# Performance work log

Hardware: AMD Instinct MI355X
Metric: run time of the kernel (lower is better)

## Reference

```python
import jax, jax.numpy as jnp
import numpy as np

B, L, D = 16, 2048, 1024  # memory_len == input_len (mask is applied on both axes)
NEG = -1e20


def setup_inputs() -> dict:
    key = jax.random.key(0)
    k1, k2, k3, k4, k5, k6 = jax.random.split(key, 6)
    inp = jax.random.normal(k1, (B, L, D), dtype=jnp.float32)
    mem = jax.random.normal(k2, (B, L, D), dtype=jnp.float32)
    # True = masked-out position; keep sparsity low so rows stay mostly valid
    mask = jax.random.bernoulli(k3, 0.1, (B, L))
    inv = 1.0 / np.sqrt(D)
    w_input = jax.random.normal(k4, (D,), dtype=jnp.float32) * inv   # Linear(D,1) weight
    w_memory = jax.random.normal(k5, (D,), dtype=jnp.float32) * inv  # Linear(D,1) weight
    dot_scale = jax.random.uniform(k6, (D,), dtype=jnp.float32, minval=0.0, maxval=inv)
    return {"input": inp, "memory": mem, "mask": mask,
            "w_input": w_input, "w_memory": w_memory, "dot_scale": dot_scale}


def reference(input, memory, mask, w_input, w_memory, dot_scale):
    # dropout p = 0.0 -> identity
    input_dot = jnp.einsum("bld,d->bl", input, w_input)[:, :, None]   # [B,L,1]
    memory_dot = jnp.einsum("bmd,d->bm", memory, w_memory)[:, None, :]  # [B,1,M]
    cross_dot = jnp.einsum("bld,bmd->blm", input * dot_scale, memory)   # [B,L,M]
    att = input_dot + memory_dot + cross_dot
    bad = mask[:, :, None] | mask[:, None, :]                           # [B,L,M]
    att = jnp.where(bad, NEG, att)
    weight_one = jax.nn.softmax(att, axis=-1)                           # over memory axis
    output_one = jnp.einsum("blm,bmd->bld", weight_one, memory)
    weight_two = jax.nn.softmax(att.max(axis=-1), axis=-1)[:, None, :]  # [B,1,L]
    output_two = jnp.einsum("bol,bld->bod", weight_two, input)          # [B,1,D]
    return jnp.concatenate(
        [input, output_one, input * output_one, output_two * output_one], axis=-1)
```

## Files before the change

### kernel.cpp

```cpp
#include <hip/hip_runtime.h>
#include <hip/hip_bf16.h>


#define BDIM 16
#define LDIM 2048
#define MDIM 2048
#define DDIM 1024
#define NEGF (-60000.0f)

typedef float    f32x4v __attribute__((ext_vector_type(4)));
typedef _Float16 half8  __attribute__((ext_vector_type(8)));
typedef _Float16 half4  __attribute__((ext_vector_type(4)));

#define GL16(gp, lp)                                                        \
  __builtin_amdgcn_global_load_lds(                                         \
      (const __attribute__((address_space(1))) unsigned int*)(gp),          \
      (__attribute__((address_space(3))) unsigned int*)(lp), 16, 0, 0)

__global__ __launch_bounds__(256) void conv_kernel(
    const float* __restrict__ input, const float* __restrict__ memory,
    const float* __restrict__ w_in, const float* __restrict__ w_mem,
    const float* __restrict__ scale,
    _Float16* __restrict__ Qh, _Float16* __restrict__ Kh,
    float* __restrict__ idot, float* __restrict__ mdot) {
  const int t = threadIdx.x, lane = t & 63, wid = t >> 6;
  const size_t row = (size_t)blockIdx.x * 4 + wid;
  const float* ir  = input  + row * DDIM;
  const float* mrp = memory + row * DDIM;
  float di = 0.f, dm = 0.f;
#pragma unroll
  for (int c = 0; c < 4; ++c) {
    const int off = c * 256 + lane * 4;
    float4 sc4 = *(const float4*)&scale[off];
    float4 wi4 = *(const float4*)&w_in[off];
    float4 wm4 = *(const float4*)&w_mem[off];
    float4 v = *(const float4*)&ir[off];
    di += v.x * wi4.x + v.y * wi4.y + v.z * wi4.z + v.w * wi4.w;
    half4 q = { (_Float16)(v.x * sc4.x), (_Float16)(v.y * sc4.y),
                (_Float16)(v.z * sc4.z), (_Float16)(v.w * sc4.w) };
    *(half4*)&Qh[row * DDIM + off] = q;
    float4 u = *(const float4*)&mrp[off];
    dm += u.x * wm4.x + u.y * wm4.y + u.z * wm4.z + u.w * wm4.w;
    half4 k = { (_Float16)u.x, (_Float16)u.y, (_Float16)u.z, (_Float16)u.w };
    *(half4*)&Kh[row * DDIM + off] = k;
  }
#pragma unroll
  for (int o = 1; o < 64; o <<= 1) {
    di += __shfl_xor(di, o, 64);
    dm += __shfl_xor(dm, o, 64);
  }
  if (lane == 0) { idot[row] = di; mdot[row] = dm; }
}

__global__ __launch_bounds__(256) void tr_kernel(const _Float16* __restrict__ Kh,
                                                 _Float16* __restrict__ Vt) {
  const int b = blockIdx.z;
  const int d0 = blockIdx.x * 64, m0 = blockIdx.y * 64;
  __shared__ _Float16 sT[64][80];
  const int t = threadIdx.x;
  {
    const int mr = t >> 2, ch = (t & 3) * 16;
    const _Float16* src = Kh + ((size_t)b * MDIM + m0 + mr) * DDIM + d0 + ch;
    *(half8*)&sT[mr][ch]     = *(const half8*)&src[0];
    *(half8*)&sT[mr][ch + 8] = *(const half8*)&src[8];
  }
  __syncthreads();
  {
    const int dr = t >> 2, mc = (t & 3) * 16;
    union { _Float16 h[16]; half8 v[2]; } tmp;
#pragma unroll
    for (int j = 0; j < 16; ++j) tmp.h[j] = sT[mc + j][dr];
    _Float16* dst = Vt + ((size_t)b * DDIM + d0 + dr) * MDIM + m0 + mc;
    *(half8*)&dst[0] = tmp.v[0];
    *(half8*)&dst[8] = tmp.v[1];
  }
}

__device__ __forceinline__ void stage128(const _Float16* __restrict__ Ab,
                                         const _Float16* __restrict__ Bb,
                                         _Float16* sAb, _Float16* sBb,
                                         int stride, int k0, int wid, int lane) {
  const int rsub = lane >> 3;
  const int sc = ((lane & 7) ^ rsub) * 8;
#pragma unroll
  for (int j = 0; j < 4; ++j) {
    const int r0 = wid * 32 + j * 8;
    const size_t go = (size_t)(r0 + rsub) * stride + k0 + sc;
    GL16(Ab + go, sAb + r0 * 64);
    GL16(Bb + go, sBb + r0 * 64);
  }
}

__device__ __forceinline__ void compute128(const _Float16* sAb, const _Float16* sBb,
                                           f32x4v acc[4][4], int wr, int wc,
                                           int lane) {
  const int l15 = lane & 15;
#pragma unroll
  for (int kk = 0; kk < 2; ++kk) {
    const int colh = ((kk * 4 + (lane >> 4)) ^ (lane & 7)) * 8;
    half8 aF[4], bF[4];
#pragma unroll
    for (int i = 0; i < 4; ++i) {
      aF[i] = *(const half8*)&sAb[(wr * 64 + i * 16 + l15) * 64 + colh];
      bF[i] = *(const half8*)&sBb[(wc * 64 + i * 16 + l15) * 64 + colh];
    }
#pragma unroll
    for (int mi = 0; mi < 4; ++mi)
#pragma unroll
      for (int ni = 0; ni < 4; ++ni)
        acc[mi][ni] = __builtin_amdgcn_mfma_f32_16x16x32_f16(aF[mi], bF[ni],
                                                             acc[mi][ni], 0, 0, 0);
  }
}

__global__ __launch_bounds__(256, 3) void gemm1_kernel(
    const _Float16* __restrict__ Qh, const _Float16* __restrict__ Kh,
    const float* __restrict__ idot, const float* __restrict__ mdot,
    const int* __restrict__ mask, _Float16* __restrict__ Sp) {
  const int id = blockIdx.x;
  const int wg = (id & 7) * 512 + (id >> 3);
  const int b = wg >> 8, rem = wg & 255, by = rem >> 4, bx = rem & 15;
  const int t = threadIdx.x, lane = t & 63, wid = t >> 6;
  const int wr = wid >> 1, wc = wid & 1;
  __shared__ _Float16 sA[128 * 64];
  __shared__ _Float16 sB[128 * 64];
  __shared__ float s_dl[128], s_dm[128];
  __shared__ int   s_ml[128], s_mm[128];
  if (t < 128) {
    s_dl[t] = idot[b * LDIM + by * 128 + t];
    s_ml[t] = mask[b * LDIM + by * 128 + t];
    s_dm[t] = mdot[b * MDIM + bx * 128 + t];
    s_mm[t] = mask[b * MDIM + bx * 128 + t];
  }
  const _Float16* Ab = Qh + ((size_t)b * LDIM + by * 128) * DDIM;
  const _Float16* Bb = Kh + ((size_t)b * MDIM + bx * 128) * DDIM;
  f32x4v acc[4][4];
#pragma unroll
  for (int i = 0; i < 4; ++i)
#pragma unroll
    for (int j = 0; j < 4; ++j) acc[i][j] = (f32x4v){0.f, 0.f, 0.f, 0.f};

  for (int ks = 0; ks < DDIM / 64; ++ks) {
    __syncthreads();
    stage128(Ab, Bb, sA, sB, DDIM, ks * 64, wid, lane);
    __syncthreads();
    compute128(sA, sB, acc, wr, wc, lane);
  }

  const int rb = wr * 64, cb = wc * 64;
#pragma unroll
  for (int mi = 0; mi < 4; ++mi)
#pragma unroll
    for (int ni = 0; ni < 4; ++ni)
#pragma unroll
      for (int r = 0; r < 4; ++r) {
        const int lrow = rb + mi * 16 + (lane >> 4) * 4 + r;
        const int lcol = cb + ni * 16 + (lane & 15);
        float s = acc[mi][ni][r] + s_dl[lrow] + s_dm[lcol];
        if ((s_ml[lrow] | s_mm[lcol]) != 0) s = NEGF;
        Sp[((size_t)b * LDIM + by * 128 + lrow) * MDIM + bx * 128 + lcol] = (_Float16)s;
      }
}

__global__ __launch_bounds__(256) void softmax_rows(_Float16* __restrict__ Sp,
                                                    float* __restrict__ rmax) {
  const int t = threadIdx.x, lane = t & 63, wid = t >> 6;
  const size_t row = (size_t)blockIdx.x * 4 + wid;
  _Float16* rp = Sp + row * (size_t)MDIM;
  float s[32];
#pragma unroll
  for (int c = 0; c < 4; ++c) {
    half8 v = *(const half8*)&rp[c * 512 + lane * 8];
#pragma unroll
    for (int j = 0; j < 8; ++j) s[c * 8 + j] = (float)v[j];
  }
  float m = -3.0e38f;
#pragma unroll
  for (int i = 0; i < 32; ++i) m = fmaxf(m, s[i]);
#pragma unroll
  for (int o = 1; o < 64; o <<= 1) m = fmaxf(m, __shfl_xor(m, o, 64));
  float sum = 0.f;
#pragma unroll
  for (int i = 0; i < 32; ++i) { s[i] = __expf(s[i] - m); sum += s[i]; }
#pragma unroll
  for (int o = 1; o < 64; o <<= 1) sum += __shfl_xor(sum, o, 64);
  const float inv = 1.f / sum;
#pragma unroll
  for (int c = 0; c < 4; ++c) {
    half8 v;
#pragma unroll
    for (int j = 0; j < 8; ++j) v[j] = (_Float16)(s[c * 8 + j] * inv);
    *(half8*)&rp[c * 512 + lane * 8] = v;
  }
  if (lane == 0) rmax[row] = m;
}

__global__ __launch_bounds__(256) void w2a_kernel(const float* __restrict__ rmax,
                                                  float* __restrict__ w2) {
  const int b = blockIdx.x, t = threadIdx.x;
  __shared__ float red[256];
  const float* rm = rmax + (size_t)b * LDIM;
  float vals[8]; float lm = -3.0e38f;
#pragma unroll
  for (int j = 0; j < 8; ++j) { vals[j] = rm[t + j * 256]; lm = fmaxf(lm, vals[j]); }
  red[t] = lm; __syncthreads();
  for (int s = 128; s > 0; s >>= 1) {
    if (t < s) red[t] = fmaxf(red[t], red[t + s]);
    __syncthreads();
  }
  const float M = red[0]; __syncthreads();
  float ls = 0.f;
#pragma unroll
  for (int j = 0; j < 8; ++j) ls += __expf(vals[j] - M);
  red[t] = ls; __syncthreads();
  for (int s = 128; s > 0; s >>= 1) {
    if (t < s) red[t] += red[t + s];
    __syncthreads();
  }
  const float inv = 1.f / red[0];
#pragma unroll
  for (int j = 0; j < 8; ++j) w2[(size_t)b * LDIM + t + j * 256] = __expf(vals[j] - M) * inv;
}

__global__ void o2init_kernel(float* __restrict__ o2) {
  o2[blockIdx.x * 256 + threadIdx.x] = 0.f;
}

__global__ __launch_bounds__(256) void o2_kernel(const float* __restrict__ input,
                                                 const float* __restrict__ w2,
                                                 float* __restrict__ o2) {
  const int b = blockIdx.y, ch = blockIdx.x, t = threadIdx.x;
  __shared__ float sw[128];
  if (t < 128) sw[t] = w2[(size_t)b * LDIM + ch * 128 + t];
  __syncthreads();
  const float* ib = input + ((size_t)b * LDIM + ch * 128) * DDIM;
  float4 acc = {0.f, 0.f, 0.f, 0.f};
  for (int l = 0; l < 128; ++l) {
    const float w = sw[l];
    float4 v = *(const float4*)&ib[(size_t)l * DDIM + t * 4];
    acc.x += w * v.x; acc.y += w * v.y; acc.z += w * v.z; acc.w += w * v.w;
  }
  atomicAdd(&o2[b * DDIM + t * 4 + 0], acc.x);
  atomicAdd(&o2[b * DDIM + t * 4 + 1], acc.y);
  atomicAdd(&o2[b * DDIM + t * 4 + 2], acc.z);
  atomicAdd(&o2[b * DDIM + t * 4 + 3], acc.w);
}

__global__ __launch_bounds__(256, 3) void gemm2_kernel(
    const _Float16* __restrict__ Pm, const _Float16* __restrict__ Vt,
    const float* __restrict__ input, const float* __restrict__ o2,
    float* __restrict__ out) {
  const int id = blockIdx.x;
  const int wg = (id & 7) * 256 + (id >> 3);
  const int b = wg >> 7, rem = wg & 127, by = rem >> 3, bx = rem & 7;
  const int t = threadIdx.x, lane = t & 63, wid = t >> 6;
  const int wr = wid >> 1, wc = wid & 1;
  __shared__ _Float16 sA[128 * 64];
  __shared__ _Float16 sB[128 * 64];
  const _Float16* Ab = Pm + ((size_t)b * LDIM + by * 128) * MDIM;
  const _Float16* Bb = Vt + ((size_t)b * DDIM + bx * 128) * MDIM;
  f32x4v acc[4][4];
#pragma unroll
  for (int i = 0; i < 4; ++i)
#pragma unroll
    for (int j = 0; j < 4; ++j) acc[i][j] = (f32x4v){0.f, 0.f, 0.f, 0.f};

  for (int ks = 0; ks < MDIM / 64; ++ks) {
    __syncthreads();
    stage128(Ab, Bb, sA, sB, MDIM, ks * 64, wid, lane);
    __syncthreads();
    compute128(sA, sB, acc, wr, wc, lane);
  }

  const int rb = wr * 64, cb = wc * 64;
#pragma unroll
  for (int mi = 0; mi < 4; ++mi)
#pragma unroll
    for (int ni = 0; ni < 4; ++ni)
#pragma unroll
      for (int r = 0; r < 4; ++r) {
        const int lrow = rb + mi * 16 + (lane >> 4) * 4 + r;
        const int lcol = cb + ni * 16 + (lane & 15);
        const size_t l = (size_t)by * 128 + lrow;
        const int d = bx * 128 + lcol;
        const float o1 = acc[mi][ni][r];
        const float inp = input[((size_t)b * LDIM + l) * DDIM + d];
        const float o2v = o2[b * DDIM + d];
        const size_t ob = ((size_t)b * LDIM + l) * (4 * DDIM) + d;
        out[ob] = inp;
        out[ob + DDIM] = o1;
        out[ob + 2 * DDIM] = inp * o1;
        out[ob + 3 * DDIM] = o2v * o1;
      }
}

extern "C" void kernel_launch(void* const* d_in, const int* in_sizes, int n_in,
                              void* d_out, int out_size, void* d_ws, size_t ws_size,
                              hipStream_t stream) {
  (void)in_sizes; (void)n_in; (void)out_size; (void)ws_size;
  const float* input  = (const float*)d_in[0];
  const float* memory = (const float*)d_in[1];
  const int*   mask   = (const int*)d_in[2];
  const float* w_in   = (const float*)d_in[3];
  const float* w_mem  = (const float*)d_in[4];
  const float* scale  = (const float*)d_in[5];
  float* out = (float*)d_out;

  char* p = (char*)d_ws;
  _Float16* Qh = (_Float16*)p; p += (size_t)BDIM * LDIM * DDIM * 2;
  _Float16* Kh = (_Float16*)p; p += (size_t)BDIM * MDIM * DDIM * 2;
  _Float16* Vt = (_Float16*)p; p += (size_t)BDIM * DDIM * MDIM * 2;
  _Float16* Sp = (_Float16*)p; p += (size_t)BDIM * LDIM * MDIM * 2;
  float* idot = (float*)p; p += (size_t)BDIM * LDIM * 4;
  float* mdot = (float*)p; p += (size_t)BDIM * MDIM * 4;
  float* rmax = (float*)p; p += (size_t)BDIM * LDIM * 4;
  float* w2   = (float*)p; p += (size_t)BDIM * LDIM * 4;
  float* o2   = (float*)p; p += (size_t)BDIM * DDIM * 4;

  conv_kernel<<<dim3(BDIM * LDIM / 4), dim3(256), 0, stream>>>(
      input, memory, w_in, w_mem, scale, Qh, Kh, idot, mdot);
  tr_kernel<<<dim3(DDIM / 64, MDIM / 64, BDIM), dim3(256), 0, stream>>>(Kh, Vt);
  gemm1_kernel<<<dim3(BDIM * 16 * 16), dim3(256), 0, stream>>>(
      Qh, Kh, idot, mdot, mask, Sp);
  softmax_rows<<<dim3(BDIM * LDIM / 4), dim3(256), 0, stream>>>(Sp, rmax);
  w2a_kernel<<<dim3(BDIM), dim3(256), 0, stream>>>(rmax, w2);
  o2init_kernel<<<dim3(BDIM * DDIM / 256), dim3(256), 0, stream>>>(o2);
  o2_kernel<<<dim3(LDIM / 128, BDIM), dim3(256), 0, stream>>>(input, w2, o2);
  gemm2_kernel<<<dim3(BDIM * 16 * 8), dim3(256), 0, stream>>>(
      Sp, Vt, input, o2, out);
}
```

Before: 653.2 us.

## Rewrite score GEMM as 256x256 tiles with triple-buffered async LDS pipeline

Result: no change. 645.4 us (-1.2%).

```diff
diff --git a/kernel.cpp b/kernel.cpp
--- a/kernel.cpp
+++ b/kernel.cpp
@@ -76,80 +76,98 @@
   }
 }
 
-__device__ __forceinline__ void stage128(const _Float16* __restrict__ Ab,
-                                         const _Float16* __restrict__ Bb,
-                                         _Float16* sAb, _Float16* sBb,
-                                         int stride, int k0, int wid, int lane) {
-  const int rsub = lane >> 3;
-  const int sc = ((lane & 7) ^ rsub) * 8;
-#pragma unroll
-  for (int j = 0; j < 4; ++j) {
-    const int r0 = wid * 32 + j * 8;
-    const size_t go = (size_t)(r0 + rsub) * stride + k0 + sc;
-    GL16(Ab + go, sAb + r0 * 64);
-    GL16(Bb + go, sBb + r0 * 64);
-  }
-}
-
-__device__ __forceinline__ void compute128(const _Float16* sAb, const _Float16* sBb,
-                                           f32x4v acc[4][4], int wr, int wc,
-                                           int lane) {
-  const int l15 = lane & 15;
-#pragma unroll
-  for (int kk = 0; kk < 2; ++kk) {
-    const int colh = ((kk * 4 + (lane >> 4)) ^ (lane & 7)) * 8;
-    half8 aF[4], bF[4];
-#pragma unroll
-    for (int i = 0; i < 4; ++i) {
-      aF[i] = *(const half8*)&sAb[(wr * 64 + i * 16 + l15) * 64 + colh];
-      bF[i] = *(const half8*)&sBb[(wc * 64 + i * 16 + l15) * 64 + colh];
-    }
-#pragma unroll
-    for (int mi = 0; mi < 4; ++mi)
-#pragma unroll
-      for (int ni = 0; ni < 4; ++ni)
-        acc[mi][ni] = __builtin_amdgcn_mfma_f32_16x16x32_f16(aF[mi], bF[ni],
-                                                             acc[mi][ni], 0, 0, 0);
-  }
-}
-
-__global__ __launch_bounds__(256, 3) void gemm1_kernel(
+__device__ __forceinline__ void stage256x32(const _Float16* __restrict__ src,
+                                            _Float16* dst, int stride, int k0,
+                                            int wid, int lane) {
+#pragma unroll
+  for (int c = 0; c < 2; ++c) {
+    const int r = c * 128 + wid * 16 + (lane >> 2);
+    const int q = (lane & 3) ^ ((r >> 1) & 3);
+    GL16(src + (size_t)r * stride + k0 + q * 8, dst + (c * 128 + wid * 16) * 32);
+  }
+}
+
+__device__ __forceinline__ half8 ldsfrag(const _Float16* s, int r, int kq) {
+  return *(const half8*)&s[r * 32 + ((kq ^ ((r >> 1) & 3)) << 3)];
+}
+
+__global__ __launch_bounds__(512, 2) void gemm1_kernel(
     const _Float16* __restrict__ Qh, const _Float16* __restrict__ Kh,
     const float* __restrict__ idot, const float* __restrict__ mdot,
     const int* __restrict__ mask, _Float16* __restrict__ Sp) {
   const int id = blockIdx.x;
-  const int wg = (id & 7) * 512 + (id >> 3);
-  const int b = wg >> 8, rem = wg & 255, by = rem >> 4, bx = rem & 15;
+  const int wg = (id & 7) * 128 + (id >> 3);
+  const int b = wg >> 6, rem = wg & 63, by = rem >> 3, bx = rem & 7;
   const int t = threadIdx.x, lane = t & 63, wid = t >> 6;
-  const int wr = wid >> 1, wc = wid & 1;
-  __shared__ _Float16 sA[128 * 64];
-  __shared__ _Float16 sB[128 * 64];
-  __shared__ float s_dl[128], s_dm[128];
-  __shared__ int   s_ml[128], s_mm[128];
-  if (t < 128) {
-    s_dl[t] = idot[b * LDIM + by * 128 + t];
-    s_ml[t] = mask[b * LDIM + by * 128 + t];
-    s_dm[t] = mdot[b * MDIM + bx * 128 + t];
-    s_mm[t] = mask[b * MDIM + bx * 128 + t];
-  }
-  const _Float16* Ab = Qh + ((size_t)b * LDIM + by * 128) * DDIM;
-  const _Float16* Bb = Kh + ((size_t)b * MDIM + bx * 128) * DDIM;
-  f32x4v acc[4][4];
-#pragma unroll
-  for (int i = 0; i < 4; ++i)
+  const int wrow = wid >> 2, wcol = wid & 3;
+  __shared__ _Float16 sA[3][256 * 32];
+  __shared__ _Float16 sB[3][256 * 32];
+  __shared__ float s_dl[256], s_dm[256];
+  __shared__ int   s_ml[256], s_mm[256];
+  if (t < 256) {
+    s_dl[t] = idot[b * LDIM + by * 256 + t];
+    s_ml[t] = mask[b * LDIM + by * 256 + t];
+    s_dm[t] = mdot[b * MDIM + bx * 256 + t];
+    s_mm[t] = mask[b * MDIM + bx * 256 + t];
+  }
+  const _Float16* Ab = Qh + ((size_t)b * LDIM + by * 256) * DDIM;
+  const _Float16* Bb = Kh + ((size_t)b * MDIM + bx * 256) * DDIM;
+  constexpr int NT = DDIM / 32;
+  f32x4v acc[8][4];
+#pragma unroll
+  for (int i = 0; i < 8; ++i)
 #pragma unroll
     for (int j = 0; j < 4; ++j) acc[i][j] = (f32x4v){0.f, 0.f, 0.f, 0.f};
 
-  for (int ks = 0; ks < DDIM / 64; ++ks) {
-    __syncthreads();
-    stage128(Ab, Bb, sA, sB, DDIM, ks * 64, wid, lane);
-    __syncthreads();
-    compute128(sA, sB, acc, wr, wc, lane);
-  }
-
-  const int rb = wr * 64, cb = wc * 64;
-#pragma unroll
-  for (int mi = 0; mi < 4; ++mi)
+  stage256x32(Ab, sA[0], DDIM, 0, wid, lane);
+  stage256x32(Bb, sB[0], DDIM, 0, wid, lane);
+  stage256x32(Ab, sA[1], DDIM, 32, wid, lane);
+  stage256x32(Bb, sB[1], DDIM, 32, wid, lane);
+  asm volatile("s_waitcnt vmcnt(4)" ::: "memory");
+  __builtin_amdgcn_s_barrier();
+
+  const int kq = lane >> 4, l15 = lane & 15;
+  int sl = 0;
+  for (int tt = 0; tt < NT; ++tt) {
+    const _Float16* cA = sA[sl];
+    const _Float16* cB = sB[sl];
+    const int sn = (sl + 2 >= 3) ? sl - 1 : sl + 2;
+    half8 aF[4], bF[4];
+#pragma unroll
+    for (int mi = 0; mi < 4; ++mi) aF[mi] = ldsfrag(cA, wrow * 128 + mi * 16 + l15, kq);
+#pragma unroll
+    for (int ni = 0; ni < 4; ++ni) bF[ni] = ldsfrag(cB, wcol * 64 + ni * 16 + l15, kq);
+    if (tt + 2 < NT) stage256x32(Ab, sA[sn], DDIM, (tt + 2) * 32, wid, lane);
+    __builtin_amdgcn_s_barrier();
+    __builtin_amdgcn_s_setprio(1);
+#pragma unroll
+    for (int mi = 0; mi < 4; ++mi)
+#pragma unroll
+      for (int ni = 0; ni < 4; ++ni)
+        acc[mi][ni] = __builtin_amdgcn_mfma_f32_16x16x32_f16(aF[mi], bF[ni], acc[mi][ni], 0, 0, 0);
+    __builtin_amdgcn_s_setprio(0);
+    __builtin_amdgcn_s_barrier();
+    half8 aG[4];
+#pragma unroll
+    for (int mi = 0; mi < 4; ++mi) aG[mi] = ldsfrag(cA, wrow * 128 + (mi + 4) * 16 + l15, kq);
+    if (tt + 2 < NT) stage256x32(Bb, sB[sn], DDIM, (tt + 2) * 32, wid, lane);
+    __builtin_amdgcn_s_barrier();
+    __builtin_amdgcn_s_setprio(1);
+#pragma unroll
+    for (int mi = 0; mi < 4; ++mi)
+#pragma unroll
+      for (int ni = 0; ni < 4; ++ni)
+        acc[mi + 4][ni] = __builtin_amdgcn_mfma_f32_16x16x32_f16(aG[mi], bF[ni], acc[mi + 4][ni], 0, 0, 0);
+    __builtin_amdgcn_s_setprio(0);
+    if (tt < NT - 2)       asm volatile("s_waitcnt vmcnt(4)" ::: "memory");
+    else if (tt == NT - 2) asm volatile("s_waitcnt vmcnt(0)" ::: "memory");
+    __builtin_amdgcn_s_barrier();
+    sl = (sl + 1 == 3) ? 0 : sl + 1;
+  }
+
+  const int rb = wrow * 128, cb = wcol * 64;
+#pragma unroll
+  for (int mi = 0; mi < 8; ++mi)
 #pragma unroll
     for (int ni = 0; ni < 4; ++ni)
 #pragma unroll
@@ -158,7 +176,7 @@
         const int lcol = cb + ni * 16 + (lane & 15);
         float s = acc[mi][ni][r] + s_dl[lrow] + s_dm[lcol];
         if ((s_ml[lrow] | s_mm[lcol]) != 0) s = NEGF;
-        Sp[((size_t)b * LDIM + by * 128 + lrow) * MDIM + bx * 128 + lcol] = (_Float16)s;
+        Sp[((size_t)b * LDIM + by * 256 + lrow) * MDIM + bx * 256 + lcol] = (_Float16)s;
       }
 }
 
@@ -196,8 +214,10 @@
 }
 
 __global__ __launch_bounds__(256) void w2a_kernel(const float* __restrict__ rmax,
-                                                  float* __restrict__ w2) {
+                                                  float* __restrict__ w2,
+                                                  float* __restrict__ o2) {
   const int b = blockIdx.x, t = threadIdx.x;
+  ((float4*)(o2 + (size_t)b * DDIM))[t] = (float4){0.f, 0.f, 0.f, 0.f};
   __shared__ float red[256];
   const float* rm = rmax + (size_t)b * LDIM;
   float vals[8]; float lm = -3.0e38f;
@@ -220,10 +240,6 @@
   const float inv = 1.f / red[0];
 #pragma unroll
   for (int j = 0; j < 8; ++j) w2[(size_t)b * LDIM + t + j * 256] = __expf(vals[j] - M) * inv;
-}
-
-__global__ void o2init_kernel(float* __restrict__ o2) {
-  o2[blockIdx.x * 256 + threadIdx.x] = 0.f;
 }
 
 __global__ __launch_bounds__(256) void o2_kernel(const float* __restrict__ input,
@@ -244,6 +260,43 @@
   atomicAdd(&o2[b * DDIM + t * 4 + 1], acc.y);
   atomicAdd(&o2[b * DDIM + t * 4 + 2], acc.z);
   atomicAdd(&o2[b * DDIM + t * 4 + 3], acc.w);
+}
+
+__device__ __forceinline__ void stage128(const _Float16* __restrict__ Ab,
+                                         const _Float16* __restrict__ Bb,
+                                         _Float16* sAb, _Float16* sBb,
+                                         int stride, int k0, int wid, int lane) {
+  const int rsub = lane >> 3;
+  const int sc = ((lane & 7) ^ rsub) * 8;
+#pragma unroll
+  for (int j = 0; j < 4; ++j) {
+    const int r0 = wid * 32 + j * 8;
+    const size_t go = (size_t)(r0 + rsub) * stride + k0 + sc;
+    GL16(Ab + go, sAb + r0 * 64);
+    GL16(Bb + go, sBb + r0 * 64);
+  }
+}
+
+__device__ __forceinline__ void compute128(const _Float16* sAb, const _Float16* sBb,
+                                           f32x4v acc[4][4], int wr, int wc,
+                                           int lane) {
+  const int l15 = lane & 15;
+#pragma unroll
+  for (int kk = 0; kk < 2; ++kk) {
+    const int colh = ((kk * 4 + (lane >> 4)) ^ (lane & 7)) * 8;
+    half8 aF[4], bF[4];
+#pragma unroll
+    for (int i = 0; i < 4; ++i) {
+      aF[i] = *(const half8*)&sAb[(wr * 64 + i * 16 + l15) * 64 + colh];
+      bF[i] = *(const half8*)&sBb[(wc * 64 + i * 16 + l15) * 64 + colh];
+    }
+#pragma unroll
+    for (int mi = 0; mi < 4; ++mi)
+#pragma unroll
+      for (int ni = 0; ni < 4; ++ni)
+        acc[mi][ni] = __builtin_amdgcn_mfma_f32_16x16x32_f16(aF[mi], bF[ni],
+                                                             acc[mi][ni], 0, 0, 0);
+  }
 }
 
 __global__ __launch_bounds__(256, 3) void gemm2_kernel(
@@ -287,10 +340,10 @@
         const float inp = input[((size_t)b * LDIM + l) * DDIM + d];
         const float o2v = o2[b * DDIM + d];
         const size_t ob = ((size_t)b * LDIM + l) * (4 * DDIM) + d;
-        out[ob] = inp;
-        out[ob + DDIM] = o1;
-        out[ob + 2 * DDIM] = inp * o1;
-        out[ob + 3 * DDIM] = o2v * o1;
+        __builtin_nontemporal_store(inp, &out[ob]);
+        __builtin_nontemporal_store(o1, &out[ob + DDIM]);
+        __builtin_nontemporal_store(inp * o1, &out[ob + 2 * DDIM]);
+        __builtin_nontemporal_store(o2v * o1, &out[ob + 3 * DDIM]);
       }
 }
 
@@ -320,11 +373,10 @@
   conv_kernel<<<dim3(BDIM * LDIM / 4), dim3(256), 0, stream>>>(
       input, memory, w_in, w_mem, scale, Qh, Kh, idot, mdot);
   tr_kernel<<<dim3(DDIM / 64, MDIM / 64, BDIM), dim3(256), 0, stream>>>(Kh, Vt);
-  gemm1_kernel<<<dim3(BDIM * 16 * 16), dim3(256), 0, stream>>>(
+  gemm1_kernel<<<dim3(BDIM * 8 * 8), dim3(512), 0, stream>>>(
       Qh, Kh, idot, mdot, mask, Sp);
   softmax_rows<<<dim3(BDIM * LDIM / 4), dim3(256), 0, stream>>>(Sp, rmax);
-  w2a_kernel<<<dim3(BDIM), dim3(256), 0, stream>>>(rmax, w2);
-  o2init_kernel<<<dim3(BDIM * DDIM / 256), dim3(256), 0, stream>>>(o2);
+  w2a_kernel<<<dim3(BDIM), dim3(256), 0, stream>>>(rmax, w2, o2);
   o2_kernel<<<dim3(LDIM / 128, BDIM), dim3(256), 0, stream>>>(input, w2, o2);
   gemm2_kernel<<<dim3(BDIM * 16 * 8), dim3(256), 0, stream>>>(
       Sp, Vt, input, o2, out);
```

## Stage GEMM epilogues through LDS for coalesced vector and nontemporal stores

Applied to the files above, without the earlier changes.

New measurement: 552.9 us (median of 2 runs). 1.18x faster.

```diff
diff --git a/kernel.cpp b/kernel.cpp
--- a/kernel.cpp
+++ b/kernel.cpp
@@ -16,6 +16,14 @@
   __builtin_amdgcn_global_load_lds(                                         \
       (const __attribute__((address_space(1))) unsigned int*)(gp),          \
       (__attribute__((address_space(3))) unsigned int*)(lp), 16, 0, 0)
+
+__device__ __forceinline__ float4 m4(const float4 a, const float4 b) {
+  return (float4){a.x * b.x, a.y * b.y, a.z * b.z, a.w * b.w};
+}
+__device__ __forceinline__ void nts4(const float4 v, float* p) {
+  f32x4v w = {v.x, v.y, v.z, v.w};
+  __builtin_nontemporal_store(w, (f32x4v*)p);
+}
 
 __global__ __launch_bounds__(256) void conv_kernel(
     const float* __restrict__ input, const float* __restrict__ memory,
@@ -113,7 +121,7 @@
   }
 }
 
-__global__ __launch_bounds__(256, 3) void gemm1_kernel(
+__global__ __launch_bounds__(256, 4) void gemm1_kernel(
     const _Float16* __restrict__ Qh, const _Float16* __restrict__ Kh,
     const float* __restrict__ idot, const float* __restrict__ mdot,
     const int* __restrict__ mask, _Float16* __restrict__ Sp) {
@@ -122,8 +130,10 @@
   const int b = wg >> 8, rem = wg & 255, by = rem >> 4, bx = rem & 15;
   const int t = threadIdx.x, lane = t & 63, wid = t >> 6;
   const int wr = wid >> 1, wc = wid & 1;
-  __shared__ _Float16 sA[128 * 64];
-  __shared__ _Float16 sB[128 * 64];
+  __shared__ union SM1 {
+    struct { _Float16 a[128 * 64]; _Float16 b[128 * 64]; } ab;
+    _Float16 s[128 * 140];
+  } sm;
   __shared__ float s_dl[128], s_dm[128];
   __shared__ int   s_ml[128], s_mm[128];
   if (t < 128) {
@@ -142,11 +152,12 @@
 
   for (int ks = 0; ks < DDIM / 64; ++ks) {
     __syncthreads();
-    stage128(Ab, Bb, sA, sB, DDIM, ks * 64, wid, lane);
-    __syncthreads();
-    compute128(sA, sB, acc, wr, wc, lane);
-  }
-
+    stage128(Ab, Bb, sm.ab.a, sm.ab.b, DDIM, ks * 64, wid, lane);
+    __syncthreads();
+    compute128(sm.ab.a, sm.ab.b, acc, wr, wc, lane);
+  }
+
+  __syncthreads();
   const int rb = wr * 64, cb = wc * 64;
 #pragma unroll
   for (int mi = 0; mi < 4; ++mi)
@@ -158,8 +169,16 @@
         const int lcol = cb + ni * 16 + (lane & 15);
         float s = acc[mi][ni][r] + s_dl[lrow] + s_dm[lcol];
         if ((s_ml[lrow] | s_mm[lcol]) != 0) s = NEGF;
-        Sp[((size_t)b * LDIM + by * 128 + lrow) * MDIM + bx * 128 + lcol] = (_Float16)s;
+        sm.s[lrow * 140 + lcol] = (_Float16)s;
       }
+  __syncthreads();
+  const int r16 = t >> 4, c8 = (t & 15) * 8;
+#pragma unroll
+  for (int rd = 0; rd < 8; ++rd) {
+    const int lrow = rd * 16 + r16;
+    half8 v = *(const half8*)&sm.s[lrow * 140 + c8];
+    *(half8*)&Sp[((size_t)b * LDIM + by * 128 + lrow) * MDIM + bx * 128 + c8] = v;
+  }
 }
 
 __global__ __launch_bounds__(256) void softmax_rows(_Float16* __restrict__ Sp,
@@ -196,8 +215,10 @@
 }
 
 __global__ __launch_bounds__(256) void w2a_kernel(const float* __restrict__ rmax,
-                                                  float* __restrict__ w2) {
+                                                  float* __restrict__ w2,
+                                                  float* __restrict__ o2) {
   const int b = blockIdx.x, t = threadIdx.x;
+  ((float4*)(o2 + (size_t)b * DDIM))[t] = (float4){0.f, 0.f, 0.f, 0.f};
   __shared__ float red[256];
   const float* rm = rmax + (size_t)b * LDIM;
   float vals[8]; float lm = -3.0e38f;
@@ -220,10 +241,6 @@
   const float inv = 1.f / red[0];
 #pragma unroll
   for (int j = 0; j < 8; ++j) w2[(size_t)b * LDIM + t + j * 256] = __expf(vals[j] - M) * inv;
-}
-
-__global__ void o2init_kernel(float* __restrict__ o2) {
-  o2[blockIdx.x * 256 + threadIdx.x] = 0.f;
 }
 
 __global__ __launch_bounds__(256) void o2_kernel(const float* __restrict__ input,
@@ -246,7 +263,7 @@
   atomicAdd(&o2[b * DDIM + t * 4 + 3], acc.w);
 }
 
-__global__ __launch_bounds__(256, 3) void gemm2_kernel(
+__global__ __launch_bounds__(256, 4) void gemm2_kernel(
     const _Float16* __restrict__ Pm, const _Float16* __restrict__ Vt,
     const float* __restrict__ input, const float* __restrict__ o2,
     float* __restrict__ out) {
@@ -255,8 +272,10 @@
   const int b = wg >> 7, rem = wg & 127, by = rem >> 3, bx = rem & 7;
   const int t = threadIdx.x, lane = t & 63, wid = t >> 6;
   const int wr = wid >> 1, wc = wid & 1;
-  __shared__ _Float16 sA[128 * 64];
-  __shared__ _Float16 sB[128 * 64];
+  __shared__ union SM2 {
+    struct { _Float16 a[128 * 64]; _Float16 b[128 * 64]; } ab;
+    float c[16 * 132];
+  } sm;
   const _Float16* Ab = Pm + ((size_t)b * LDIM + by * 128) * MDIM;
   const _Float16* Bb = Vt + ((size_t)b * DDIM + bx * 128) * MDIM;
   f32x4v acc[4][4];
@@ -267,31 +286,45 @@
 
   for (int ks = 0; ks < MDIM / 64; ++ks) {
     __syncthreads();
-    stage128(Ab, Bb, sA, sB, MDIM, ks * 64, wid, lane);
-    __syncthreads();
-    compute128(sA, sB, acc, wr, wc, lane);
-  }
-
-  const int rb = wr * 64, cb = wc * 64;
-#pragma unroll
-  for (int mi = 0; mi < 4; ++mi)
-#pragma unroll
-    for (int ni = 0; ni < 4; ++ni)
-#pragma unroll
-      for (int r = 0; r < 4; ++r) {
-        const int lrow = rb + mi * 16 + (lane >> 4) * 4 + r;
-        const int lcol = cb + ni * 16 + (lane & 15);
-        const size_t l = (size_t)by * 128 + lrow;
-        const int d = bx * 128 + lcol;
-        const float o1 = acc[mi][ni][r];
-        const float inp = input[((size_t)b * LDIM + l) * DDIM + d];
-        const float o2v = o2[b * DDIM + d];
-        const size_t ob = ((size_t)b * LDIM + l) * (4 * DDIM) + d;
-        out[ob] = inp;
-        out[ob + DDIM] = o1;
-        out[ob + 2 * DDIM] = inp * o1;
-        out[ob + 3 * DDIM] = o2v * o1;
-      }
+    stage128(Ab, Bb, sm.ab.a, sm.ab.b, MDIM, ks * 64, wid, lane);
+    __syncthreads();
+    compute128(sm.ab.a, sm.ab.b, acc, wr, wc, lane);
+  }
+
+  const int cq = (t & 15) * 4;
+  const float4 o2a = *(const float4*)&o2[b * DDIM + bx * 128 + cq];
+  const float4 o2b = *(const float4*)&o2[b * DDIM + bx * 128 + 64 + cq];
+  const int r16 = t >> 4;
+  __syncthreads();
+#pragma unroll
+  for (int pp = 0; pp < 8; ++pp) {
+    if (wr == (pp >> 2)) {
+      const int pmi = pp & 3;
+#pragma unroll
+      for (int ni = 0; ni < 4; ++ni)
+#pragma unroll
+        for (int r = 0; r < 4; ++r)
+          sm.c[((lane >> 4) * 4 + r) * 132 + wc * 64 + ni * 16 + (lane & 15)] =
+              acc[pmi][ni][r];
+    }
+    __syncthreads();
+    const size_t l = (size_t)by * 128 + pp * 16 + r16;
+    const float4 c0 = *(const float4*)&sm.c[r16 * 132 + cq];
+    const float4 c1 = *(const float4*)&sm.c[r16 * 132 + 64 + cq];
+    const float* ibp = &input[((size_t)b * LDIM + l) * DDIM + bx * 128];
+    const float4 i0 = *(const float4*)&ibp[cq];
+    const float4 i1 = *(const float4*)&ibp[64 + cq];
+    float* ob = &out[((size_t)b * LDIM + l) * (4 * DDIM) + bx * 128];
+    nts4(i0, ob + cq);
+    nts4(i1, ob + 64 + cq);
+    nts4(c0, ob + DDIM + cq);
+    nts4(c1, ob + DDIM + 64 + cq);
+    nts4(m4(i0, c0), ob + 2 * DDIM + cq);
+    nts4(m4(i1, c1), ob + 2 * DDIM + 64 + cq);
+    nts4(m4(o2a, c0), ob + 3 * DDIM + cq);
+    nts4(m4(o2b, c1), ob + 3 * DDIM + 64 + cq);
+    __syncthreads();
+  }
 }
 
 extern "C" void kernel_launch(void* const* d_in, const int* in_sizes, int n_in,
@@ -323,8 +356,7 @@
   gemm1_kernel<<<dim3(BDIM * 16 * 16), dim3(256), 0, stream>>>(
       Qh, Kh, idot, mdot, mask, Sp);
   softmax_rows<<<dim3(BDIM * LDIM / 4), dim3(256), 0, stream>>>(Sp, rmax);
-  w2a_kernel<<<dim3(BDIM), dim3(256), 0, stream>>>(rmax, w2);
-  o2init_kernel<<<dim3(BDIM * DDIM / 256), dim3(256), 0, stream>>>(o2);
+  w2a_kernel<<<dim3(BDIM), dim3(256), 0, stream>>>(rmax, w2, o2);
   o2_kernel<<<dim3(LDIM / 128, BDIM), dim3(256), 0, stream>>>(input, w2, o2);
   gemm2_kernel<<<dim3(BDIM * 16 * 8), dim3(256), 0, stream>>>(
       Sp, Vt, input, o2, out);
```
